# Optimization experiments

Hardware: AMD Instinct MI355X
Metric: run time of the kernel (lower is better)

The kernel has to match this reference:

```python
import jax, jax.numpy as jnp
import numpy as np

EPS = 1e-8  # matches torch F.cosine_similarity eps


def setup_inputs() -> dict:
    key = jax.random.key(0)
    S, U, D = 2048, 10, 256  # speakers, utterances/speaker, embedding dim
    embeddings = jax.random.normal(key, (S * U, D), dtype=jnp.float32)
    labels = jnp.repeat(jnp.arange(S, dtype=jnp.int64), U)  # speaker-blocked, as the view() assumes
    return {"embeddings": embeddings, "labels": labels}


def reference(embeddings, labels):
    labels_np = np.asarray(labels)
    S = int(np.unique(labels_np).size)          # num_speakers (static)
    B, D = embeddings.shape
    U = B // S                                   # num_utterances
    E = embeddings.reshape(S, U, D)
    C = E.mean(axis=1)                           # (S, D) centroids
    En = E / jnp.maximum(jnp.linalg.norm(E, axis=-1, keepdims=True), EPS)
    Cn = C / jnp.maximum(jnp.linalg.norm(C, axis=-1, keepdims=True), EPS)
    sim = jnp.einsum('sud,kd->suk', En, Cn)      # (S, U, S) cosine similarities
    idx = jnp.arange(S)
    pos = sim[idx, :, idx]                       # (S, U) similarity to own centroid
    neg_mask = jnp.eye(S, dtype=bool)[:, None, :]  # mask out k == i
    neg = jnp.where(neg_mask, -jnp.inf, sim)
    lse = jax.nn.logsumexp(neg, axis=-1)         # (S, U)
    loss = jnp.mean(-pos + lse)
    return loss
```

## Files before the change

### kernel.cpp

```cpp
#include <hip/hip_runtime.h>
#include <math.h>

#define SS   2048
#define UU   10
#define DD   256
#define BB   (SS * UU)
#define EPSF 1e-8f

typedef __attribute__((ext_vector_type(8))) short   bf16x8;
typedef __attribute__((ext_vector_type(4))) float   floatx4;

__device__ static inline unsigned short f2bf(float f) {
    union { float f; unsigned u; } v; v.f = f;
    unsigned r = (v.u + 0x7FFFu + ((v.u >> 16) & 1u)) >> 16;
    return (unsigned short)r;
}

__device__ static inline void gl_lds16(const unsigned short* g, unsigned short* l) {
    __builtin_amdgcn_global_load_lds((const __attribute__((address_space(1))) void*)g,
                                     (__attribute__((address_space(3))) void*)l, 16, 0, 0);
}

__global__ __launch_bounds__(256) void normalize_kernel(const float* __restrict__ E,
                                                        unsigned short* __restrict__ Enb) {
    const int wid = threadIdx.x >> 6, lane = threadIdx.x & 63;
    const int row = blockIdx.x * 4 + wid;
    float4 v = ((const float4*)(E + (size_t)row * DD))[lane];
    float ss = v.x * v.x + v.y * v.y + v.z * v.z + v.w * v.w;
#pragma unroll
    for (int off = 32; off; off >>= 1) ss += __shfl_xor(ss, off, 64);
    const float rinv = 1.0f / fmaxf(sqrtf(ss), EPSF);
    ushort4 o;
    o.x = f2bf(v.x * rinv); o.y = f2bf(v.y * rinv);
    o.z = f2bf(v.z * rinv); o.w = f2bf(v.w * rinv);
    ((ushort4*)(Enb + (size_t)row * DD))[lane] = o;
}

__global__ __launch_bounds__(256) void centroid_kernel(const float* __restrict__ E,
                                                       unsigned short* __restrict__ Cnb) {
    const int s = blockIdx.x, d = threadIdx.x;
    const float* base = E + (size_t)s * UU * DD + d;
    float c = 0.f;
#pragma unroll
    for (int u = 0; u < UU; ++u) c += base[u * DD];
    c *= 0.1f;
    __shared__ float sred[256];
    sred[d] = c * c;
    __syncthreads();
#pragma unroll
    for (int off = 128; off; off >>= 1) {
        if (d < off) sred[d] += sred[d + off];
        __syncthreads();
    }
    const float rinv = 1.0f / fmaxf(sqrtf(sred[0]), EPSF);
    Cnb[(size_t)s * DD + d] = f2bf(c * rinv);
}

#define BM 128
#define BN 128
#define BK 32

__global__ __launch_bounds__(256) void gemm_lse_kernel(const unsigned short* __restrict__ Enb,
                                                       const unsigned short* __restrict__ Cnb,
                                                       float* __restrict__ posArr,
                                                       float* __restrict__ sumexp) {
    __shared__ unsigned short As[BM * BK];
    __shared__ unsigned short Bs[BN * BK];

    const int tid  = threadIdx.x;
    const int wid  = tid >> 6, lane = tid & 63;
    const int l15  = lane & 15, quad = lane >> 4;
    const int wave_m = wid >> 1, wave_n = wid & 1;

    const int bn = blockIdx.x & 15;
    const int bm = blockIdx.x >> 4;
    const int row0 = bm * BM, n0 = bn * BN;

    const int chunk = wid * 2;
    const unsigned short* gA0 = Enb + (size_t)(row0 + chunk * 16 + (lane >> 2)) * DD + (lane & 3) * 8;
    const unsigned short* gB0 = Cnb + (size_t)(n0   + chunk * 16 + (lane >> 2)) * DD + (lane & 3) * 8;
    unsigned short* lA0 = As + chunk * 512;
    unsigned short* lB0 = Bs + chunk * 512;

    int aoff[4], boff[4];
#pragma unroll
    for (int t = 0; t < 4; ++t) {
        aoff[t] = (wave_m * 64 + t * 16 + l15) * BK + quad * 8;
        boff[t] = (wave_n * 64 + t * 16 + l15) * BK + quad * 8;
    }

    floatx4 acc[4][4];
#pragma unroll
    for (int i = 0; i < 4; ++i)
#pragma unroll
        for (int j = 0; j < 4; ++j) acc[i][j] = (floatx4){0.f, 0.f, 0.f, 0.f};

    for (int k0 = 0; k0 < DD; k0 += BK) {
        __syncthreads();
        gl_lds16(gA0 + k0,            lA0);
        gl_lds16(gA0 + k0 + 16 * DD,  lA0 + 512);
        gl_lds16(gB0 + k0,            lB0);
        gl_lds16(gB0 + k0 + 16 * DD,  lB0 + 512);
        __syncthreads();

        bf16x8 af[4], bfr[4];
#pragma unroll
        for (int t = 0; t < 4; ++t) af[t]  = *(const bf16x8*)(As + aoff[t]);
#pragma unroll
        for (int t = 0; t < 4; ++t) bfr[t] = *(const bf16x8*)(Bs + boff[t]);
#pragma unroll
        for (int mt = 0; mt < 4; ++mt)
#pragma unroll
            for (int nt = 0; nt < 4; ++nt)
                acc[mt][nt] = __builtin_amdgcn_mfma_f32_16x16x32_bf16(af[mt], bfr[nt], acc[mt][nt], 0, 0, 0);
    }

#pragma unroll
    for (int mt = 0; mt < 4; ++mt) {
        float rs[4] = {0.f, 0.f, 0.f, 0.f};
        const int growb = row0 + wave_m * 64 + mt * 16 + quad * 4;
#pragma unroll
        for (int nt = 0; nt < 4; ++nt) {
            const int col = n0 + wave_n * 64 + nt * 16 + l15;
#pragma unroll
            for (int r = 0; r < 4; ++r) {
                const int grow = growb + r;
                const float sim = acc[mt][nt][r];
                if (col == grow / UU) {
                    posArr[grow] = sim;
                } else {
                    rs[r] += __expf(sim);
                }
            }
        }
#pragma unroll
        for (int m = 1; m < 16; m <<= 1) {
#pragma unroll
            for (int r = 0; r < 4; ++r) rs[r] += __shfl_xor(rs[r], m, 64);
        }
        if (l15 == 0) {
#pragma unroll
            for (int r = 0; r < 4; ++r) atomicAdd(&sumexp[growb + r], rs[r]);
        }
    }
}

__global__ __launch_bounds__(256) void finalize_kernel(const float* __restrict__ posArr,
                                                       const float* __restrict__ sumexp,
                                                       float* __restrict__ out) {
    __shared__ float sred[256];
    const int tid = threadIdx.x;
    float t = 0.f;
    for (int r = tid; r < BB; r += 256) t += logf(sumexp[r]) - posArr[r];
    sred[tid] = t;
    __syncthreads();
#pragma unroll
    for (int off = 128; off; off >>= 1) {
        if (tid < off) sred[tid] += sred[tid + off];
        __syncthreads();
    }
    if (tid == 0) out[0] = sred[0] / (float)BB;
}

extern "C" void kernel_launch(void* const* d_in, const int* in_sizes, int n_in,
                              void* d_out, int out_size, void* d_ws, size_t ws_size,
                              hipStream_t stream) {
    const float* E = (const float*)d_in[0];
    float* out = (float*)d_out;

    unsigned short* Enb = (unsigned short*)d_ws;
    unsigned short* Cnb = Enb + (size_t)BB * DD;
    float* posArr = (float*)(Cnb + (size_t)SS * DD);
    float* sumexp = posArr + BB;

    hipMemsetAsync(sumexp, 0, BB * sizeof(float), stream);

    normalize_kernel<<<BB / 4, 256, 0, stream>>>(E, Enb);
    centroid_kernel<<<SS, 256, 0, stream>>>(E, Cnb);
    gemm_lse_kernel<<<(BB / BM) * (SS / BN), 256, 0, stream>>>(Enb, Cnb, posArr, sumexp);
    finalize_kernel<<<1, 256, 0, stream>>>(posArr, sumexp, out);
}
```

Measured before the change: 141.7 us.

## Fuse normalize and centroid prep, enlarge GEMM tile with swizzled LDS, widen finalize

Result: faster. 122.2 us (-13.8%).

```diff
diff --git a/kernel.cpp b/kernel.cpp
--- a/kernel.cpp
+++ b/kernel.cpp
@@ -21,30 +21,36 @@
                                      (__attribute__((address_space(3))) void*)l, 16, 0, 0);
 }
 
-__global__ __launch_bounds__(256) void normalize_kernel(const float* __restrict__ E,
-                                                        unsigned short* __restrict__ Enb) {
+__global__ __launch_bounds__(256) void prep_kernel(const float* __restrict__ E,
+                                                   unsigned short* __restrict__ Enb,
+                                                   unsigned short* __restrict__ Cnb) {
+    const int s   = blockIdx.x;
     const int wid = threadIdx.x >> 6, lane = threadIdx.x & 63;
-    const int row = blockIdx.x * 4 + wid;
-    float4 v = ((const float4*)(E + (size_t)row * DD))[lane];
-    float ss = v.x * v.x + v.y * v.y + v.z * v.z + v.w * v.w;
+    __shared__ float cent[4][256];
+    __shared__ float sred[256];
+
+    float cp0 = 0.f, cp1 = 0.f, cp2 = 0.f, cp3 = 0.f;
+    for (int u = wid; u < UU; u += 4) {
+        const size_t roff = (size_t)(s * UU + u) * DD;
+        float4 v = ((const float4*)(E + roff))[lane];
+        float ssq = v.x * v.x + v.y * v.y + v.z * v.z + v.w * v.w;
 #pragma unroll
-    for (int off = 32; off; off >>= 1) ss += __shfl_xor(ss, off, 64);
-    const float rinv = 1.0f / fmaxf(sqrtf(ss), EPSF);
-    ushort4 o;
-    o.x = f2bf(v.x * rinv); o.y = f2bf(v.y * rinv);
-    o.z = f2bf(v.z * rinv); o.w = f2bf(v.w * rinv);
-    ((ushort4*)(Enb + (size_t)row * DD))[lane] = o;
-}
+        for (int off = 32; off; off >>= 1) ssq += __shfl_xor(ssq, off, 64);
+        const float rinv = 1.0f / fmaxf(sqrtf(ssq), EPSF);
+        ushort4 o;
+        o.x = f2bf(v.x * rinv); o.y = f2bf(v.y * rinv);
+        o.z = f2bf(v.z * rinv); o.w = f2bf(v.w * rinv);
+        ((ushort4*)(Enb + roff))[lane] = o;
+        cp0 += v.x; cp1 += v.y; cp2 += v.z; cp3 += v.w;
+    }
+    cent[wid][lane * 4 + 0] = cp0;
+    cent[wid][lane * 4 + 1] = cp1;
+    cent[wid][lane * 4 + 2] = cp2;
+    cent[wid][lane * 4 + 3] = cp3;
+    __syncthreads();
 
-__global__ __launch_bounds__(256) void centroid_kernel(const float* __restrict__ E,
-                                                       unsigned short* __restrict__ Cnb) {
-    const int s = blockIdx.x, d = threadIdx.x;
-    const float* base = E + (size_t)s * UU * DD + d;
-    float c = 0.f;
-#pragma unroll
-    for (int u = 0; u < UU; ++u) c += base[u * DD];
-    c *= 0.1f;
-    __shared__ float sred[256];
+    const int d = threadIdx.x;
+    const float c = (cent[0][d] + cent[1][d] + cent[2][d] + cent[3][d]) * 0.1f;
     sred[d] = c * c;
     __syncthreads();
 #pragma unroll
@@ -56,14 +62,14 @@
     Cnb[(size_t)s * DD + d] = f2bf(c * rinv);
 }
 
-#define BM 128
+#define BM 256
 #define BN 128
-#define BK 32
+#define BK 64
 
-__global__ __launch_bounds__(256) void gemm_lse_kernel(const unsigned short* __restrict__ Enb,
-                                                       const unsigned short* __restrict__ Cnb,
-                                                       float* __restrict__ posArr,
-                                                       float* __restrict__ sumexp) {
+__global__ __launch_bounds__(256, 2) void gemm_lse_kernel(const unsigned short* __restrict__ Enb,
+                                                          const unsigned short* __restrict__ Cnb,
+                                                          float* __restrict__ posArr,
+                                                          float* __restrict__ sumexp) {
     __shared__ unsigned short As[BM * BK];
     __shared__ unsigned short Bs[BN * BK];
 
@@ -76,49 +82,60 @@
     const int bm = blockIdx.x >> 4;
     const int row0 = bm * BM, n0 = bn * BN;
 
-    const int chunk = wid * 2;
-    const unsigned short* gA0 = Enb + (size_t)(row0 + chunk * 16 + (lane >> 2)) * DD + (lane & 3) * 8;
-    const unsigned short* gB0 = Cnb + (size_t)(n0   + chunk * 16 + (lane >> 2)) * DD + (lane & 3) * 8;
-    unsigned short* lA0 = As + chunk * 512;
-    unsigned short* lB0 = Bs + chunk * 512;
-
-    int aoff[4], boff[4];
+    const int rl  = lane >> 3;
+    const int gl8 = ((lane & 7) ^ rl) * 8;
+    const unsigned short* gp[12];
+    unsigned short* lp[12];
 #pragma unroll
-    for (int t = 0; t < 4; ++t) {
-        aoff[t] = (wave_m * 64 + t * 16 + l15) * BK + quad * 8;
-        boff[t] = (wave_n * 64 + t * 16 + l15) * BK + quad * 8;
+    for (int i = 0; i < 12; ++i) {
+        const int c = wid * 12 + i;
+        if (c < 32) {
+            gp[i] = Enb + (size_t)(row0 + c * 8 + rl) * DD + gl8;
+            lp[i] = As + c * 512;
+        } else {
+            gp[i] = Cnb + (size_t)(n0 + (c - 32) * 8 + rl) * DD + gl8;
+            lp[i] = Bs + (c - 32) * 512;
+        }
     }
 
-    floatx4 acc[4][4];
+    const int swz8 = ((quad ^ (l15 & 7))) * 8;
+    int aoff[8], boff[4];
 #pragma unroll
-    for (int i = 0; i < 4; ++i)
+    for (int mt = 0; mt < 8; ++mt) aoff[mt] = (wave_m * 128 + mt * 16 + l15) * BK + swz8;
+#pragma unroll
+    for (int nt = 0; nt < 4; ++nt) boff[nt] = (wave_n * 64 + nt * 16 + l15) * BK + swz8;
+
+    floatx4 acc[8][4];
+#pragma unroll
+    for (int i = 0; i < 8; ++i)
 #pragma unroll
         for (int j = 0; j < 4; ++j) acc[i][j] = (floatx4){0.f, 0.f, 0.f, 0.f};
 
     for (int k0 = 0; k0 < DD; k0 += BK) {
         __syncthreads();
-        gl_lds16(gA0 + k0,            lA0);
-        gl_lds16(gA0 + k0 + 16 * DD,  lA0 + 512);
-        gl_lds16(gB0 + k0,            lB0);
-        gl_lds16(gB0 + k0 + 16 * DD,  lB0 + 512);
+#pragma unroll
+        for (int i = 0; i < 12; ++i) gl_lds16(gp[i] + k0, lp[i]);
         __syncthreads();
-
-        bf16x8 af[4], bfr[4];
 #pragma unroll
-        for (int t = 0; t < 4; ++t) af[t]  = *(const bf16x8*)(As + aoff[t]);
+        for (int ks = 0; ks < 2; ++ks) {
+            const int kx = ks * 32;
+            bf16x8 af[8], bfr[4];
 #pragma unroll
-        for (int t = 0; t < 4; ++t) bfr[t] = *(const bf16x8*)(Bs + boff[t]);
+            for (int mt = 0; mt < 8; ++mt) af[mt]  = *(const bf16x8*)(As + (aoff[mt] ^ kx));
 #pragma unroll
-        for (int mt = 0; mt < 4; ++mt)
+            for (int nt = 0; nt < 4; ++nt) bfr[nt] = *(const bf16x8*)(Bs + (boff[nt] ^ kx));
 #pragma unroll
-            for (int nt = 0; nt < 4; ++nt)
-                acc[mt][nt] = __builtin_amdgcn_mfma_f32_16x16x32_bf16(af[mt], bfr[nt], acc[mt][nt], 0, 0, 0);
+            for (int mt = 0; mt < 8; ++mt)
+#pragma unroll
+                for (int nt = 0; nt < 4; ++nt)
+                    acc[mt][nt] = __builtin_amdgcn_mfma_f32_16x16x32_bf16(af[mt], bfr[nt], acc[mt][nt], 0, 0, 0);
+        }
     }
 
 #pragma unroll
-    for (int mt = 0; mt < 4; ++mt) {
+    for (int mt = 0; mt < 8; ++mt) {
         float rs[4] = {0.f, 0.f, 0.f, 0.f};
-        const int growb = row0 + wave_m * 64 + mt * 16 + quad * 4;
+        const int growb = row0 + wave_m * 128 + mt * 16 + quad * 4;
 #pragma unroll
         for (int nt = 0; nt < 4; ++nt) {
             const int col = n0 + wave_n * 64 + nt * 16 + l15;
@@ -145,17 +162,17 @@
     }
 }
 
-__global__ __launch_bounds__(256) void finalize_kernel(const float* __restrict__ posArr,
-                                                       const float* __restrict__ sumexp,
-                                                       float* __restrict__ out) {
-    __shared__ float sred[256];
+__global__ __launch_bounds__(1024) void finalize_kernel(const float* __restrict__ posArr,
+                                                        const float* __restrict__ sumexp,
+                                                        float* __restrict__ out) {
+    __shared__ float sred[1024];
     const int tid = threadIdx.x;
     float t = 0.f;
-    for (int r = tid; r < BB; r += 256) t += logf(sumexp[r]) - posArr[r];
+    for (int r = tid; r < BB; r += 1024) t += logf(sumexp[r]) - posArr[r];
     sred[tid] = t;
     __syncthreads();
 #pragma unroll
-    for (int off = 128; off; off >>= 1) {
+    for (int off = 512; off; off >>= 1) {
         if (tid < off) sred[tid] += sred[tid + off];
         __syncthreads();
     }
@@ -175,8 +192,7 @@
 
     hipMemsetAsync(sumexp, 0, BB * sizeof(float), stream);
 
-    normalize_kernel<<<BB / 4, 256, 0, stream>>>(E, Enb);
-    centroid_kernel<<<SS, 256, 0, stream>>>(E, Cnb);
+    prep_kernel<<<SS, 256, 0, stream>>>(E, Enb, Cnb);
     gemm_lse_kernel<<<(BB / BM) * (SS / BN), 256, 0, stream>>>(Enb, Cnb, posArr, sumexp);
-    finalize_kernel<<<1, 256, 0, stream>>>(posArr, sumexp, out);
+    finalize_kernel<<<1, 1024, 0, stream>>>(posArr, sumexp, out);
 }
```
